# Performance work log

Hardware: AMD Instinct MI355X
Metric: run time of the kernel (lower is better)

The kernel has to match this reference:

```python
import jax, jax.numpy as jnp
import numpy as np

H = 1024      # hidden_size
I = 4096      # expert_intermediate_size (4*H)
E = 8         # num_experts (routed)
K = 2         # num_experts_per_token
SHARED = 1    # shared experts
LB_W = 0.01   # load_balance_loss_weight
Z_W = 0.01    # router z-loss weight
INIT_STD = 0.02


def _expert_mlp(x, gate_w, up_w, down_w):
    # SwiGLU expert: down( silu(x @ gate^T) * (x @ up^T) )
    return (jax.nn.silu(x @ gate_w.T) * (x @ up_w.T)) @ down_w.T


def setup_inputs() -> dict:
    key = jax.random.key(0)
    ks = jax.random.split(key, 8)
    f32 = jnp.float32
    return {
        'hidden_states': jax.random.normal(ks[0], (2, 2048, H), f32),
        'router_w': jax.random.normal(ks[1], (E, H), f32) * INIT_STD,
        'gate_w': jax.random.normal(ks[2], (E, I, H), f32) * INIT_STD,
        'up_w': jax.random.normal(ks[3], (E, I, H), f32) * INIT_STD,
        'down_w': jax.random.normal(ks[4], (E, H, I), f32) * INIT_STD,
        'sh_gate_w': jax.random.normal(ks[5], (I, H), f32) * INIT_STD,
        'sh_up_w': jax.random.normal(ks[6], (I, H), f32) * INIT_STD,
        'sh_down_w': jax.random.normal(ks[7], (H, I), f32) * INIT_STD,
    }


def reference(hidden_states, router_w, gate_w, up_w, down_w, sh_gate_w, sh_up_w, sh_down_w):
    B, S, Hd = hidden_states.shape
    x = hidden_states.reshape(-1, Hd)            # [T, H]
    T = x.shape[0]

    # Router (identity pre-router net, no bias)
    router_logits = x @ router_w.T               # [T, E]
    router_probs = jax.nn.softmax(router_logits, axis=-1)
    routing_weights, selected_experts = jax.lax.top_k(router_probs, K)  # [T, K]
    routing_weights = routing_weights / routing_weights.sum(-1, keepdims=True)

    # Per-token per-expert combine weights: sum_k w_k * [sel_k == e]
    onehot = jax.nn.one_hot(selected_experts, E, dtype=routing_weights.dtype)  # [T, K, E]
    combine = jnp.einsum('tk,tke->te', routing_weights, onehot)               # [T, E]

    # Routed experts (fixed small loop over E experts, vectorized over tokens)
    expert_out = jnp.zeros_like(x)
    for e in range(E):
        y = _expert_mlp(x, gate_w[e], up_w[e], down_w[e])                     # [T, H]
        expert_out = expert_out + y * combine[:, e:e + 1]

    # Shared expert(s) (SHARED == 1): averaged dense expert applied to all tokens
    shared_out = _expert_mlp(x, sh_gate_w, sh_up_w, sh_down_w) / SHARED

    final = (expert_out + shared_out).reshape(B, S, Hd)

    # Aux losses
    routed_mask = (onehot.sum(1) > 0).astype(jnp.float32)                     # [T, E]
    loads = jnp.concatenate([routed_mask.sum(0),
                             jnp.full((SHARED,), float(T), jnp.float32)])     # [E+SHARED]
    loads_n = loads / loads.sum()
    ideal = 1.0 / (E + SHARED)
    load_balance_loss = jnp.mean((loads_n - ideal) ** 2)
    router_z_loss = jnp.mean(jnp.sum(router_logits ** 2, axis=-1))
    total_aux_loss = LB_W * load_balance_loss + Z_W * router_z_loss
    return final, total_aux_loss
```

## Files before the change

kernel.cpp:

```cpp
#include <hip/hip_runtime.h>


typedef unsigned short u16;
typedef unsigned int u32;

typedef short bf16x8 __attribute__((ext_vector_type(8)));
typedef float f32x4 __attribute__((ext_vector_type(4)));

#define GLD16(g, l)                                                            \
  __builtin_amdgcn_global_load_lds(                                            \
      (const __attribute__((address_space(1))) void*)(g),                      \
      (__attribute__((address_space(3))) void*)(l), 16, 0, 0)

__device__ __forceinline__ u32 rne16(float f) {
  u32 u = __float_as_uint(f);
  return (u + 0x7fffu + ((u >> 16) & 1u)) >> 16;
}
__device__ __forceinline__ u16 bf16of(float f) { return (u16)rne16(f); }
__device__ __forceinline__ u32 pk2(float lo, float hi) {
  return rne16(lo) | (rne16(hi) << 16);
}


__global__ void zero_meta_kernel(int* __restrict__ meta) {
  int t = threadIdx.x;
  if (t < 8) meta[t] = 0;
  if (t == 8) ((float*)(meta + 32))[0] = 0.0f;
}

__global__ void router_kernel(const float* __restrict__ x,
                              const float* __restrict__ rw,
                              u16* __restrict__ xb, int* __restrict__ tlist,
                              float* __restrict__ gwv, int* __restrict__ meta) {
  int tok = blockIdx.x;
  int lane = threadIdx.x;
  const float* xr = x + (size_t)tok * 1024;
  float acc[8] = {0.f, 0.f, 0.f, 0.f, 0.f, 0.f, 0.f, 0.f};
#pragma unroll
  for (int c = 0; c < 16; c++) {
    float xv = xr[lane + 64 * c];
    xb[(size_t)tok * 1024 + lane + 64 * c] = bf16of(xv);
#pragma unroll
    for (int e = 0; e < 8; e++) acc[e] += xv * rw[e * 1024 + lane + 64 * c];
  }
#pragma unroll
  for (int e = 0; e < 8; e++) {
    float v = acc[e];
    for (int m = 32; m > 0; m >>= 1) v += __shfl_xor(v, m, 64);
    acc[e] = v;
  }
  if (lane == 0) {
    float z = 0.f;
#pragma unroll
    for (int e = 0; e < 8; e++) z += acc[e] * acc[e];
    atomicAdd((float*)(meta + 32), z);
    int i1 = 0;
    float b1 = acc[0];
#pragma unroll
    for (int e = 1; e < 8; e++)
      if (acc[e] > b1) { b1 = acc[e]; i1 = e; }
    int i2 = -1;
    float b2 = -3.0e38f;
#pragma unroll
    for (int e = 0; e < 8; e++)
      if (e != i1 && acc[e] > b2) { b2 = acc[e]; i2 = e; }
    float w1 = 1.0f / (1.0f + __expf(b2 - b1));
    float w2 = 1.0f - w1;
    int s1 = atomicAdd(&meta[i1], 1);
    tlist[i1 * 4096 + s1] = tok;
    gwv[i1 * 4096 + s1] = w1;
    int s2 = atomicAdd(&meta[i2], 1);
    tlist[i2 * 4096 + s2] = tok;
    gwv[i2 * 4096 + s2] = w2;
  }
}

__global__ void finalize_kernel(int* __restrict__ meta, float* __restrict__ out) {
  if (threadIdx.x == 0) {
    int* basep = meta + 16;
    int base = 0;
    float lb = 0.f;
    const float invsum = 1.0f / 12288.0f;
    const float ideal = 1.0f / 9.0f;
    for (int e = 0; e < 8; e++) {
      int c = meta[e];
      int p = (c + 127) & ~127;
      meta[8 + e] = p;
      basep[e] = base;
      base += p;
      float d = (float)c * invsum - ideal;
      lb += d * d;
    }
    basep[8] = base;
    float dsh = 4096.0f * invsum - ideal;
    lb += dsh * dsh;
    lb *= (1.0f / 9.0f);
    float z = ((float*)(meta + 32))[0] * (1.0f / 4096.0f);
    out[4194304] = 0.01f * lb + 0.01f * z;
  }
}

__global__ void gather_kernel(const u16* __restrict__ xb, u16* __restrict__ Ag,
                              const int* __restrict__ tlist,
                              const int* __restrict__ meta) {
  int r = blockIdx.x;
  int t = threadIdx.x;
  const int* base = meta + 16;
  int total = base[8];
  uint4 val = make_uint4(0u, 0u, 0u, 0u);
  if (r < total) {
    int e = 0;
#pragma unroll
    for (int q = 1; q < 8; q++)
      if (r >= base[q]) e = q;
    int s = r - base[e];
    if (s < meta[e]) {
      int tok = tlist[e * 4096 + s];
      val = *((const uint4*)(xb + (size_t)tok * 1024) + t);
    }
  }
  *((uint4*)(Ag + (size_t)r * 1024) + t) = val;
}

__global__ void conv_kernel(const float* __restrict__ src, u16* __restrict__ dst,
                            int n8) {
  int i = blockIdx.x * 256 + threadIdx.x;
  if (i >= n8) return;
  const float4* s = (const float4*)src + (size_t)i * 2;
  float4 a = s[0], b = s[1];
  uint4 o;
  o.x = pk2(a.x, a.y);
  o.y = pk2(a.z, a.w);
  o.z = pk2(b.x, b.y);
  o.w = pk2(b.z, b.w);
  ((uint4*)dst)[i] = o;
}

__global__ __launch_bounds__(256, 2) void gemm1_kernel(
    const u16* __restrict__ A, const u16* __restrict__ Wg,
    const u16* __restrict__ Wu, u16* __restrict__ Hout,
    const int* __restrict__ meta, int e_lo, int e_hi) {
  __shared__ u16 sA[128 * 32];
  __shared__ u16 sBg[128 * 32];
  __shared__ u16 sBu[128 * 32];

  int r0, elocal;
  if (meta != nullptr) {
    const int* base = meta + 16;
    r0 = base[e_lo] + blockIdx.y * 128;
    if (r0 >= base[e_hi]) return;
    int e = e_lo;
#pragma unroll
    for (int q = 1; q < 8; q++)
      if (q > e_lo && q < e_hi && r0 >= base[q]) e = q;
    elocal = e - e_lo;
  } else {
    r0 = blockIdx.y * 128;
    elocal = 0;
  }
  int n0 = blockIdx.x * 128;
  int t = threadIdx.x;

  const u16* aP = A + (size_t)(r0 + (t >> 2)) * 1024 + (t & 3) * 8;
  const u16* gP =
      Wg + (size_t)elocal * 4194304 + (size_t)(n0 + (t >> 2)) * 1024 + (t & 3) * 8;
  const u16* uP =
      Wu + (size_t)elocal * 4194304 + (size_t)(n0 + (t >> 2)) * 1024 + (t & 3) * 8;
  u16* aD = sA + t * 8;
  u16* gD = sBg + t * 8;
  u16* uD = sBu + t * 8;

  int lane = t & 63, wid = t >> 6;
  int wm = wid >> 1, wn = wid & 1;
  int l15 = lane & 15, quad = lane >> 4;
  const u16* aR = sA + (wm * 64 + l15) * 32 + quad * 8;
  const u16* gR = sBg + (wn * 64 + l15) * 32 + quad * 8;
  const u16* uR = sBu + (wn * 64 + l15) * 32 + quad * 8;

  f32x4 accg[4][4] = {};
  f32x4 accu[4][4] = {};

#pragma unroll 1
  for (int kk = 0; kk < 32; kk++) {
    if (kk) __syncthreads();
    GLD16(aP, aD);
    GLD16(aP + 64 * 1024, aD + 2048);
    GLD16(gP, gD);
    GLD16(gP + 64 * 1024, gD + 2048);
    GLD16(uP, uD);
    GLD16(uP + 64 * 1024, uD + 2048);
    aP += 32;
    gP += 32;
    uP += 32;
    __syncthreads();

    bf16x8 af[4];
#pragma unroll
    for (int i = 0; i < 4; i++) af[i] = *(const bf16x8*)(aR + i * 512);
#pragma unroll
    for (int j = 0; j < 4; j++) {
      bf16x8 bg = *(const bf16x8*)(gR + j * 512);
      bf16x8 bu = *(const bf16x8*)(uR + j * 512);
#pragma unroll
      for (int i = 0; i < 4; i++) {
        accg[i][j] =
            __builtin_amdgcn_mfma_f32_16x16x32_bf16(af[i], bg, accg[i][j], 0, 0, 0);
        accu[i][j] =
            __builtin_amdgcn_mfma_f32_16x16x32_bf16(af[i], bu, accu[i][j], 0, 0, 0);
      }
    }
  }

#pragma unroll
  for (int i = 0; i < 4; i++) {
    int row = r0 + wm * 64 + i * 16 + quad * 4;
#pragma unroll
    for (int r = 0; r < 4; r++) {
      u16* hrow = Hout + (size_t)(row + r) * 4096 + n0 + wn * 64 + l15;
#pragma unroll
      for (int j = 0; j < 4; j++) {
        float g = accg[i][j][r];
        float u = accu[i][j][r];
        float s = g / (1.0f + __expf(-g));
        hrow[j * 16] = bf16of(s * u);
      }
    }
  }
}

__global__ __launch_bounds__(256, 2) void gemm2_kernel(
    const u16* __restrict__ A, const u16* __restrict__ Wd,
    float* __restrict__ out, const int* __restrict__ meta, int e_lo, int e_hi,
    const int* __restrict__ tlist, const float* __restrict__ gwv, int ksteps) {
  __shared__ u16 sA[128 * 32];
  __shared__ u16 sB[128 * 32];

  int r0, e;
  if (meta != nullptr) {
    const int* base = meta + 16;
    r0 = base[e_lo] + blockIdx.y * 128;
    if (r0 >= base[e_hi]) return;
    e = e_lo;
#pragma unroll
    for (int q = 1; q < 8; q++)
      if (q > e_lo && q < e_hi && r0 >= base[q]) e = q;
  } else {
    r0 = blockIdx.y * 128;
    e = e_lo;
  }
  int elocal = e - e_lo;
  int n0 = blockIdx.x * 128;
  int k0 = blockIdx.z * ksteps;
  int t = threadIdx.x;

  const u16* aP =
      A + (size_t)(r0 + (t >> 2)) * 4096 + (size_t)k0 * 32 + (t & 3) * 8;
  const u16* bP = Wd + (size_t)elocal * 4194304 +
                  (size_t)(n0 + (t >> 2)) * 4096 + (size_t)k0 * 32 + (t & 3) * 8;
  u16* aD = sA + t * 8;
  u16* bD = sB + t * 8;

  int lane = t & 63, wid = t >> 6;
  int wm = wid >> 1, wn = wid & 1;
  int l15 = lane & 15, quad = lane >> 4;
  const u16* aR = sA + (wm * 64 + l15) * 32 + quad * 8;
  const u16* bR = sB + (wn * 64 + l15) * 32 + quad * 8;

  f32x4 acc[4][4] = {};

#pragma unroll 1
  for (int kk = 0; kk < ksteps; kk++) {
    if (kk) __syncthreads();
    GLD16(aP, aD);
    GLD16(aP + 64 * 4096, aD + 2048);
    GLD16(bP, bD);
    GLD16(bP + 64 * 4096, bD + 2048);
    aP += 32;
    bP += 32;
    __syncthreads();

    bf16x8 af[4];
#pragma unroll
    for (int i = 0; i < 4; i++) af[i] = *(const bf16x8*)(aR + i * 512);
#pragma unroll
    for (int j = 0; j < 4; j++) {
      bf16x8 bb = *(const bf16x8*)(bR + j * 512);
#pragma unroll
      for (int i = 0; i < 4; i++)
        acc[i][j] =
            __builtin_amdgcn_mfma_f32_16x16x32_bf16(af[i], bb, acc[i][j], 0, 0, 0);
    }
  }

  if (meta != nullptr) {
    int cnt_e = meta[e];
    int base_e = (meta + 16)[e];
#pragma unroll
    for (int i = 0; i < 4; i++) {
#pragma unroll
      for (int r = 0; r < 4; r++) {
        int s = r0 - base_e + wm * 64 + i * 16 + quad * 4 + r;
        if (s < cnt_e) {
          int tok = tlist[e * 4096 + s];
          float w = gwv[e * 4096 + s];
          float* orow = out + (size_t)tok * 1024 + n0 + wn * 64 + l15;
#pragma unroll
          for (int j = 0; j < 4; j++) unsafeAtomicAdd(orow + j * 16, w * acc[i][j][r]);
        }
      }
    }
  } else {
#pragma unroll
    for (int i = 0; i < 4; i++) {
#pragma unroll
      for (int r = 0; r < 4; r++) {
        int tok = r0 + wm * 64 + i * 16 + quad * 4 + r;
        float* orow = out + (size_t)tok * 1024 + n0 + wn * 64 + l15;
#pragma unroll
        for (int j = 0; j < 4; j++) orow[j * 16] = acc[i][j][r];
      }
    }
  }
}

extern "C" void kernel_launch(void* const* d_in, const int* in_sizes, int n_in,
                              void* d_out, int out_size, void* d_ws,
                              size_t ws_size, hipStream_t stream) {
  const float* x = (const float*)d_in[0];
  const float* rw = (const float*)d_in[1];
  const float* gw_ = (const float*)d_in[2];
  const float* uw_ = (const float*)d_in[3];
  const float* dw_ = (const float*)d_in[4];
  const float* sg = (const float*)d_in[5];
  const float* su = (const float*)d_in[6];
  const float* sd = (const float*)d_in[7];
  float* out = (float*)d_out;
  char* ws = (char*)d_ws;

  int* meta = (int*)(ws + 0);
  int* tlist = (int*)(ws + 256);
  float* gwv = (float*)(ws + 131328);
  u16* xb = (u16*)(ws + 262400);
  u16* Ag = (u16*)(ws + 8651008);
  u16* Hb = (u16*)(ws + 27525376);
  u16* Wbuf = (u16*)(ws + 103022848);

  int ne = 4;
  if (ws_size < 170131712ULL) ne = 2;
  if (ws_size < 136577280ULL) ne = 1;
  const size_t EW = 4194304;

  zero_meta_kernel<<<1, 64, 0, stream>>>(meta);
  router_kernel<<<4096, 64, 0, stream>>>(x, rw, xb, tlist, gwv, meta);
  finalize_kernel<<<1, 64, 0, stream>>>(meta, out);
  gather_kernel<<<9216, 128, 0, stream>>>(xb, Ag, tlist, meta);

  conv_kernel<<<2048, 256, 0, stream>>>(sg, Wbuf, 524288);
  conv_kernel<<<2048, 256, 0, stream>>>(su, Wbuf + EW, 524288);
  gemm1_kernel<<<dim3(32, 32), 256, 0, stream>>>(xb, Wbuf, Wbuf + EW, Hb,
                                                 nullptr, 0, 0);
  conv_kernel<<<2048, 256, 0, stream>>>(sd, Wbuf, 524288);
  gemm2_kernel<<<dim3(8, 32, 1), 256, 0, stream>>>(Hb, Wbuf, out, nullptr, 0, 0,
                                                   tlist, gwv, 128);

  for (int g = 0; g < 8; g += ne) {
    conv_kernel<<<ne * 2048, 256, 0, stream>>>(gw_ + (size_t)g * EW, Wbuf,
                                               ne * 524288);
    conv_kernel<<<ne * 2048, 256, 0, stream>>>(uw_ + (size_t)g * EW,
                                               Wbuf + (size_t)ne * EW,
                                               ne * 524288);
    gemm1_kernel<<<dim3(32, 72), 256, 0, stream>>>(
        Ag, Wbuf, Wbuf + (size_t)ne * EW, Hb, meta, g, g + ne);
  }

  int ne2 = 2 * ne;
  if (ne2 > 8) ne2 = 8;
  for (int g = 0; g < 8; g += ne2) {
    conv_kernel<<<ne2 * 2048, 256, 0, stream>>>(dw_ + (size_t)g * EW, Wbuf,
                                                ne2 * 524288);
    gemm2_kernel<<<dim3(8, 72, 2), 256, 0, stream>>>(Hb, Wbuf, out, meta, g,
                                                     g + ne2, tlist, gwv, 64);
  }
}
```

Before: 1.097 ms.

## Fuse fp32-to-bf16 weight conversion into GEMMs and merge shared expert into grouped launches

```diff
diff --git a/kernel.cpp b/kernel.cpp
--- a/kernel.cpp
+++ b/kernel.cpp
@@ -1,4 +1,5 @@
 #include <hip/hip_runtime.h>
+#include <hip/hip_bf16.h>
 
 
 typedef unsigned short u16;
@@ -18,7 +19,8 @@
 }
 __device__ __forceinline__ u16 bf16of(float f) { return (u16)rne16(f); }
 __device__ __forceinline__ u32 pk2(float lo, float hi) {
-  return rne16(lo) | (rne16(hi) << 16);
+  __hip_bfloat162 h = __float22bfloat162_rn(float2{lo, hi});
+  return *(u32*)&h;
 }
 
 
@@ -26,6 +28,11 @@
   int t = threadIdx.x;
   if (t < 8) meta[t] = 0;
   if (t == 8) ((float*)(meta + 32))[0] = 0.0f;
+}
+
+__global__ void zero_out_kernel(float* __restrict__ out) {
+  int i = blockIdx.x * 256 + threadIdx.x;
+  ((float4*)out)[i] = make_float4(0.f, 0.f, 0.f, 0.f);
 }
 
 __global__ void router_kernel(const float* __restrict__ x,
@@ -92,6 +99,7 @@
       lb += d * d;
     }
     basep[8] = base;
+    basep[9] = base + 4096;
     float dsh = 4096.0f * invsum - ideal;
     lb += dsh * dsh;
     lb *= (1.0f / 9.0f);
@@ -106,9 +114,13 @@
   int r = blockIdx.x;
   int t = threadIdx.x;
   const int* base = meta + 16;
-  int total = base[8];
   uint4 val = make_uint4(0u, 0u, 0u, 0u);
-  if (r < total) {
+  if (r >= base[8]) {
+    if (r < base[9]) {
+      int tok = r - base[8];
+      val = *((const uint4*)(xb + (size_t)tok * 1024) + t);
+    }
+  } else {
     int e = 0;
 #pragma unroll
     for (int q = 1; q < 8; q++)
@@ -122,53 +134,46 @@
   *((uint4*)(Ag + (size_t)r * 1024) + t) = val;
 }
 
-__global__ void conv_kernel(const float* __restrict__ src, u16* __restrict__ dst,
-                            int n8) {
-  int i = blockIdx.x * 256 + threadIdx.x;
-  if (i >= n8) return;
-  const float4* s = (const float4*)src + (size_t)i * 2;
-  float4 a = s[0], b = s[1];
-  uint4 o;
-  o.x = pk2(a.x, a.y);
-  o.y = pk2(a.z, a.w);
-  o.z = pk2(b.x, b.y);
-  o.w = pk2(b.z, b.w);
-  ((uint4*)dst)[i] = o;
-}
-
-__global__ __launch_bounds__(256, 2) void gemm1_kernel(
-    const u16* __restrict__ A, const u16* __restrict__ Wg,
-    const u16* __restrict__ Wu, u16* __restrict__ Hout,
-    const int* __restrict__ meta, int e_lo, int e_hi) {
+__global__ __launch_bounds__(256, 4) void gemm1_kernel(
+    const u16* __restrict__ A, const float* __restrict__ gw,
+    const float* __restrict__ uw, const float* __restrict__ sg,
+    const float* __restrict__ su, u16* __restrict__ Hout,
+    const int* __restrict__ meta) {
   __shared__ u16 sA[128 * 32];
   __shared__ u16 sBg[128 * 32];
   __shared__ u16 sBu[128 * 32];
 
-  int r0, elocal;
-  if (meta != nullptr) {
-    const int* base = meta + 16;
-    r0 = base[e_lo] + blockIdx.y * 128;
-    if (r0 >= base[e_hi]) return;
-    int e = e_lo;
-#pragma unroll
-    for (int q = 1; q < 8; q++)
-      if (q > e_lo && q < e_hi && r0 >= base[q]) e = q;
-    elocal = e - e_lo;
+  int bid = blockIdx.x;
+  int xcd = bid & 7;
+  int slot = bid >> 3;
+  int n_hi = slot / 104;
+  int y = slot - n_hi * 104;
+  int n0 = (n_hi * 8 + xcd) << 7;
+
+  const int* base = meta + 16;
+  int r0 = y << 7;
+  if (r0 >= base[9]) return;
+  int e = 0;
+#pragma unroll
+  for (int q = 1; q < 9; q++)
+    if (r0 >= base[q]) e = q;
+  const float *gptr, *uptr;
+  if (e == 8) {
+    gptr = sg;
+    uptr = su;
   } else {
-    r0 = blockIdx.y * 128;
-    elocal = 0;
-  }
-  int n0 = blockIdx.x * 128;
+    gptr = gw + (size_t)e * 4194304;
+    uptr = uw + (size_t)e * 4194304;
+  }
+
   int t = threadIdx.x;
-
   const u16* aP = A + (size_t)(r0 + (t >> 2)) * 1024 + (t & 3) * 8;
-  const u16* gP =
-      Wg + (size_t)elocal * 4194304 + (size_t)(n0 + (t >> 2)) * 1024 + (t & 3) * 8;
-  const u16* uP =
-      Wu + (size_t)elocal * 4194304 + (size_t)(n0 + (t >> 2)) * 1024 + (t & 3) * 8;
   u16* aD = sA + t * 8;
-  u16* gD = sBg + t * 8;
-  u16* uD = sBu + t * 8;
+  int brow = t >> 1, bcol = (t & 1) << 4;
+  const float* gP = gptr + (size_t)(n0 + brow) * 1024 + bcol;
+  const float* uP = uptr + (size_t)(n0 + brow) * 1024 + bcol;
+  uint4* gD = (uint4*)(sBg + brow * 32 + bcol);
+  uint4* uD = (uint4*)(sBu + brow * 32 + bcol);
 
   int lane = t & 63, wid = t >> 6;
   int wm = wid >> 1, wn = wid & 1;
@@ -185,13 +190,26 @@
     if (kk) __syncthreads();
     GLD16(aP, aD);
     GLD16(aP + 64 * 1024, aD + 2048);
-    GLD16(gP, gD);
-    GLD16(gP + 64 * 1024, gD + 2048);
-    GLD16(uP, uD);
-    GLD16(uP + 64 * 1024, uD + 2048);
     aP += 32;
+    float4 g0 = ((const float4*)gP)[0], g1 = ((const float4*)gP)[1];
+    float4 g2 = ((const float4*)gP)[2], g3 = ((const float4*)gP)[3];
+    float4 v0 = ((const float4*)uP)[0], v1 = ((const float4*)uP)[1];
+    float4 v2 = ((const float4*)uP)[2], v3 = ((const float4*)uP)[3];
     gP += 32;
     uP += 32;
+    uint4 pa, pb;
+    pa.x = pk2(g0.x, g0.y); pa.y = pk2(g0.z, g0.w);
+    pa.z = pk2(g1.x, g1.y); pa.w = pk2(g1.z, g1.w);
+    pb.x = pk2(g2.x, g2.y); pb.y = pk2(g2.z, g2.w);
+    pb.z = pk2(g3.x, g3.y); pb.w = pk2(g3.z, g3.w);
+    gD[0] = pa;
+    gD[1] = pb;
+    pa.x = pk2(v0.x, v0.y); pa.y = pk2(v0.z, v0.w);
+    pa.z = pk2(v1.x, v1.y); pa.w = pk2(v1.z, v1.w);
+    pb.x = pk2(v2.x, v2.y); pb.y = pk2(v2.z, v2.w);
+    pb.z = pk2(v3.x, v3.y); pb.w = pk2(v3.z, v3.w);
+    uD[0] = pa;
+    uD[1] = pb;
     __syncthreads();
 
     bf16x8 af[4];
@@ -228,37 +246,37 @@
   }
 }
 
-__global__ __launch_bounds__(256, 2) void gemm2_kernel(
-    const u16* __restrict__ A, const u16* __restrict__ Wd,
-    float* __restrict__ out, const int* __restrict__ meta, int e_lo, int e_hi,
-    const int* __restrict__ tlist, const float* __restrict__ gwv, int ksteps) {
+__global__ __launch_bounds__(256, 5) void gemm2_kernel(
+    const u16* __restrict__ A, const float* __restrict__ dw,
+    const float* __restrict__ sd, float* __restrict__ out,
+    const int* __restrict__ meta, const int* __restrict__ tlist,
+    const float* __restrict__ gwv) {
   __shared__ u16 sA[128 * 32];
   __shared__ u16 sB[128 * 32];
 
-  int r0, e;
-  if (meta != nullptr) {
-    const int* base = meta + 16;
-    r0 = base[e_lo] + blockIdx.y * 128;
-    if (r0 >= base[e_hi]) return;
-    e = e_lo;
-#pragma unroll
-    for (int q = 1; q < 8; q++)
-      if (q > e_lo && q < e_hi && r0 >= base[q]) e = q;
-  } else {
-    r0 = blockIdx.y * 128;
-    e = e_lo;
-  }
-  int elocal = e - e_lo;
-  int n0 = blockIdx.x * 128;
-  int k0 = blockIdx.z * ksteps;
+  int bid = blockIdx.x;
+  int xcd = bid & 7;
+  int slot = bid >> 3;
+  int z = slot / 104;
+  int y = slot - z * 104;
+  int n0 = xcd << 7;
+  int k0 = z << 11;
+
+  const int* base = meta + 16;
+  int r0 = y << 7;
+  if (r0 >= base[9]) return;
+  int e = 0;
+#pragma unroll
+  for (int q = 1; q < 9; q++)
+    if (r0 >= base[q]) e = q;
+  const float* dptr = (e == 8) ? sd : dw + (size_t)e * 4194304;
+
   int t = threadIdx.x;
-
-  const u16* aP =
-      A + (size_t)(r0 + (t >> 2)) * 4096 + (size_t)k0 * 32 + (t & 3) * 8;
-  const u16* bP = Wd + (size_t)elocal * 4194304 +
-                  (size_t)(n0 + (t >> 2)) * 4096 + (size_t)k0 * 32 + (t & 3) * 8;
+  const u16* aP = A + (size_t)(r0 + (t >> 2)) * 4096 + k0 + (t & 3) * 8;
   u16* aD = sA + t * 8;
-  u16* bD = sB + t * 8;
+  int brow = t >> 1, bcol = (t & 1) << 4;
+  const float* bP = dptr + (size_t)(n0 + brow) * 4096 + k0 + bcol;
+  uint4* bD = (uint4*)(sB + brow * 32 + bcol);
 
   int lane = t & 63, wid = t >> 6;
   int wm = wid >> 1, wn = wid & 1;
@@ -269,14 +287,21 @@
   f32x4 acc[4][4] = {};
 
 #pragma unroll 1
-  for (int kk = 0; kk < ksteps; kk++) {
+  for (int kk = 0; kk < 64; kk++) {
     if (kk) __syncthreads();
     GLD16(aP, aD);
     GLD16(aP + 64 * 4096, aD + 2048);
-    GLD16(bP, bD);
-    GLD16(bP + 64 * 4096, bD + 2048);
     aP += 32;
+    float4 b0 = ((const float4*)bP)[0], b1 = ((const float4*)bP)[1];
+    float4 b2 = ((const float4*)bP)[2], b3 = ((const float4*)bP)[3];
     bP += 32;
+    uint4 pa, pb2;
+    pa.x = pk2(b0.x, b0.y); pa.y = pk2(b0.z, b0.w);
+    pa.z = pk2(b1.x, b1.y); pa.w = pk2(b1.z, b1.w);
+    pb2.x = pk2(b2.x, b2.y); pb2.y = pk2(b2.z, b2.w);
+    pb2.z = pk2(b3.x, b3.y); pb2.w = pk2(b3.z, b3.w);
+    bD[0] = pa;
+    bD[1] = pb2;
     __syncthreads();
 
     bf16x8 af[4];
@@ -292,9 +317,20 @@
     }
   }
 
-  if (meta != nullptr) {
+  if (e == 8) {
+#pragma unroll
+    for (int i = 0; i < 4; i++) {
+#pragma unroll
+      for (int r = 0; r < 4; r++) {
+        int tok = r0 - base[8] + wm * 64 + i * 16 + quad * 4 + r;
+        float* orow = out + (size_t)tok * 1024 + n0 + wn * 64 + l15;
+#pragma unroll
+        for (int j = 0; j < 4; j++) unsafeAtomicAdd(orow + j * 16, acc[i][j][r]);
+      }
+    }
+  } else {
     int cnt_e = meta[e];
-    int base_e = (meta + 16)[e];
+    int base_e = base[e];
 #pragma unroll
     for (int i = 0; i < 4; i++) {
 #pragma unroll
@@ -305,19 +341,9 @@
           float w = gwv[e * 4096 + s];
           float* orow = out + (size_t)tok * 1024 + n0 + wn * 64 + l15;
 #pragma unroll
-          for (int j = 0; j < 4; j++) unsafeAtomicAdd(orow + j * 16, w * acc[i][j][r]);
+          for (int j = 0; j < 4; j++)
+            unsafeAtomicAdd(orow + j * 16, w * acc[i][j][r]);
         }
-      }
-    }
-  } else {
-#pragma unroll
-    for (int i = 0; i < 4; i++) {
-#pragma unroll
-      for (int r = 0; r < 4; r++) {
-        int tok = r0 + wm * 64 + i * 16 + quad * 4 + r;
-        float* orow = out + (size_t)tok * 1024 + n0 + wn * 64 + l15;
-#pragma unroll
-        for (int j = 0; j < 4; j++) orow[j * 16] = acc[i][j][r];
       }
     }
   }
@@ -342,43 +368,14 @@
   float* gwv = (float*)(ws + 131328);
   u16* xb = (u16*)(ws + 262400);
   u16* Ag = (u16*)(ws + 8651008);
-  u16* Hb = (u16*)(ws + 27525376);
-  u16* Wbuf = (u16*)(ws + 103022848);
-
-  int ne = 4;
-  if (ws_size < 170131712ULL) ne = 2;
-  if (ws_size < 136577280ULL) ne = 1;
-  const size_t EW = 4194304;
+  u16* Hb = (u16*)(ws + 35913984);
 
   zero_meta_kernel<<<1, 64, 0, stream>>>(meta);
+  zero_out_kernel<<<4096, 256, 0, stream>>>(out);
   router_kernel<<<4096, 64, 0, stream>>>(x, rw, xb, tlist, gwv, meta);
   finalize_kernel<<<1, 64, 0, stream>>>(meta, out);
-  gather_kernel<<<9216, 128, 0, stream>>>(xb, Ag, tlist, meta);
-
-  conv_kernel<<<2048, 256, 0, stream>>>(sg, Wbuf, 524288);
-  conv_kernel<<<2048, 256, 0, stream>>>(su, Wbuf + EW, 524288);
-  gemm1_kernel<<<dim3(32, 32), 256, 0, stream>>>(xb, Wbuf, Wbuf + EW, Hb,
-                                                 nullptr, 0, 0);
-  conv_kernel<<<2048, 256, 0, stream>>>(sd, Wbuf, 524288);
-  gemm2_kernel<<<dim3(8, 32, 1), 256, 0, stream>>>(Hb, Wbuf, out, nullptr, 0, 0,
-                                                   tlist, gwv, 128);
-
-  for (int g = 0; g < 8; g += ne) {
-    conv_kernel<<<ne * 2048, 256, 0, stream>>>(gw_ + (size_t)g * EW, Wbuf,
-                                               ne * 524288);
-    conv_kernel<<<ne * 2048, 256, 0, stream>>>(uw_ + (size_t)g * EW,
-                                               Wbuf + (size_t)ne * EW,
-                                               ne * 524288);
-    gemm1_kernel<<<dim3(32, 72), 256, 0, stream>>>(
-        Ag, Wbuf, Wbuf + (size_t)ne * EW, Hb, meta, g, g + ne);
-  }
-
-  int ne2 = 2 * ne;
-  if (ne2 > 8) ne2 = 8;
-  for (int g = 0; g < 8; g += ne2) {
-    conv_kernel<<<ne2 * 2048, 256, 0, stream>>>(dw_ + (size_t)g * EW, Wbuf,
-                                                ne2 * 524288);
-    gemm2_kernel<<<dim3(8, 72, 2), 256, 0, stream>>>(Hb, Wbuf, out, meta, g,
-                                                     g + ne2, tlist, gwv, 64);
-  }
-}
+  gather_kernel<<<13312, 128, 0, stream>>>(xb, Ag, tlist, meta);
+
+  gemm1_kernel<<<3328, 256, 0, stream>>>(Ag, gw_, uw_, sg, su, Hb, meta);
+  gemm2_kernel<<<1664, 256, 0, stream>>>(Hb, dw_, sd, out, meta, tlist, gwv);
+}
```

Measured after the change: 2.300 ms. 2.1x slower.
